# Kernel tuning notes

Measured on AMD Instinct MI355X. Metric: run time of the kernel, lower is better.

The kernel has to match this reference:

```python
import jax, jax.numpy as jnp
import numpy as np

N, E, B = 20000, 100000, 16
U_SZ, U_RED = 4096, 256
EDGE_H, EDGE_OUT = 1024, 512
NODE_H = 512
X_DIM, EA_DIM = 9, 1


def _lin(key, fan_out, fan_in):
    kw, kb = jax.random.split(key)
    s = 1.0 / np.sqrt(fan_in)
    w = jax.random.uniform(kw, (fan_out, fan_in), jnp.float32, -s, s)
    b = jax.random.uniform(kb, (fan_out,), jnp.float32, -s, s)
    return w, b


def setup_inputs() -> dict:
    key = jax.random.key(0)
    ks = jax.random.split(key, 16)
    inp = {}
    inp["x"] = jax.random.normal(ks[0], (N, X_DIM), jnp.float32)
    inp["edge_index"] = jax.random.randint(ks[1], (2, E), 0, N, jnp.int64)
    inp["edge_attr"] = jax.random.normal(ks[2], (E, EA_DIM), jnp.float32)
    inp["u"] = jax.random.normal(ks[3], (B, U_SZ), jnp.float32)
    inp["batch"] = jnp.sort(jax.random.randint(ks[4], (N,), 0, B, jnp.int64))
    # select_dim_reduction: Linear(4096, 256)
    inp["w_sel"], inp["b_sel"] = _lin(ks[5], U_RED, U_SZ)
    # edge MLP: 275 -> 1024 -> 1024 -> 1024 -> 1024 -> 512
    e_in = EA_DIM + 2 * X_DIM + U_RED  # 275
    inp["ew0"], inp["eb0"] = _lin(ks[6], EDGE_H, e_in)
    inp["ew1"], inp["eb1"] = _lin(ks[7], EDGE_H, EDGE_H)
    inp["ew2"], inp["eb2"] = _lin(ks[8], EDGE_H, EDGE_H)
    inp["ew3"], inp["eb3"] = _lin(ks[9], EDGE_H, EDGE_H)
    inp["ew4"], inp["eb4"] = _lin(ks[10], EDGE_OUT, EDGE_H)
    # node_mlp_1: (9+512) -> 512 -> 512 (relu after each)
    inp["nw0"], inp["nb0"] = _lin(ks[11], NODE_H, X_DIM + EDGE_OUT)
    inp["nw1"], inp["nb1"] = _lin(ks[12], NODE_H, NODE_H)
    # node_mlp_2: (9+512+256) -> 512 -> 1
    inp["mw0"], inp["mb0"] = _lin(ks[13], NODE_H, X_DIM + NODE_H + U_RED)
    inp["mw1"], inp["mb1"] = _lin(ks[14], 1, NODE_H)
    return inp


def reference(x, edge_index, edge_attr, u, batch,
              w_sel, b_sel,
              ew0, eb0, ew1, eb1, ew2, eb2, ew3, eb3, ew4, eb4,
              nw0, nb0, nw1, nb1, mw0, mb0, mw1, mb1):
    row, col = edge_index[0], edge_index[1]
    u_r = u @ w_sel.T + b_sel                       # [B, 256]
    eb_idx = batch[row]                             # edge -> graph
    # EdgeModel: cat([src, dest, edge_attr, u[batch]]) -> MLP
    e_in = jnp.concatenate([x[row], x[col], edge_attr, u_r[eb_idx]], axis=1)  # [E,275]
    h = jax.nn.relu(e_in @ ew0.T + eb0)
    h = jax.nn.relu(h @ ew1.T + eb1)
    h = jax.nn.relu(h @ ew2.T + eb2)
    h = jax.nn.relu(h @ ew3.T + eb3)
    edge_out = h @ ew4.T + eb4                      # [E, 512]
    # NodeModel: gather x[col], edge MLP, scatter_mean onto row
    n_in = jnp.concatenate([x[col], edge_out], axis=1)  # [E, 521]
    h = jax.nn.relu(n_in @ nw0.T + nb0)
    h = jax.nn.relu(h @ nw1.T + nb1)                # [E, 512]
    seg_sum = jax.ops.segment_sum(h, row, num_segments=x.shape[0])
    cnt = jax.ops.segment_sum(jnp.ones((h.shape[0],), h.dtype), row, num_segments=x.shape[0])
    agg = seg_sum / jnp.maximum(cnt, 1.0)[:, None]  # scatter_mean
    m_in = jnp.concatenate([x, agg, u_r[batch]], axis=1)  # [N, 777]
    h2 = jax.nn.relu(m_in @ mw0.T + mb0)
    out = h2 @ mw1.T + mb1                          # [N, 1]
    return jnp.squeeze(out)
```

## Files before the change

### kernel.cpp

```cpp
#include <hip/hip_runtime.h>


#define NN 20000
#define EE 100000
#define BB 16

typedef _Float16 f16x8 __attribute__((ext_vector_type(8)));
typedef _Float16 f16x4 __attribute__((ext_vector_type(4)));
typedef float f32x4 __attribute__((ext_vector_type(4)));

__device__ __forceinline__ int clampi(int v, int hi) {
    return v < 0 ? 0 : (v >= hi ? hi - 1 : v);
}

__device__ __forceinline__ void gld_lds16(const void* g, void* l) {
    __builtin_amdgcn_global_load_lds(
        (const __attribute__((address_space(1))) unsigned int*)g,
        (__attribute__((address_space(3))) unsigned int*)l, 16, 0, 0);
}

__global__ __launch_bounds__(512, 2) void gemm256(
    const _Float16* __restrict__ Ag, const _Float16* __restrict__ Wt,
    int KT, int KTs, const float* __restrict__ bias,
    _Float16* __restrict__ C, int KTo, int ktOff)
{
    __shared__ _Float16 As[32768];
    __shared__ _Float16 Bs[32768];

    const int tid  = threadIdx.x;
    const int lane = tid & 63;
    const int wid  = tid >> 6;
    const int wm = wid & 1;
    const int wn = wid >> 1;
    const int l15 = lane & 15;
    const int l4  = (lane >> 4) << 2;

    const int nb = gridDim.x;
    const int MT2 = gridDim.y;
    int f = blockIdx.y * nb + blockIdx.x;
    const int MT8 = MT2 & ~7;
    int p, c;
    if (f < MT8 * nb) {
        c = (f >> 3) % nb;
        p = (f & 7) + 8 * ((f >> 3) / nb);
    } else {
        int g = f - MT8 * nb;
        p = MT8 + g / nb;
        c = g % nb;
    }

    const int KTT = KT >> 1;
    const size_t soff = (size_t)tid * 8;
    const int doff = (tid & ~63) * 8;
    const int aoff = wm * 4096 + ((lane >> 4) << 10) + l15 * 8;
    const int boff = (wn >> 1) * 4096 + ((lane >> 4) << 10)
                   + ((wn & 1) * 64 + l15) * 8;

    auto stageA = [&](int tn, int s) {
        const size_t kk = (size_t)(2 * tn + s);
        const _Float16* g0 = Ag + ((size_t)(2 * p)     * KTs + kk) * 4096 + soff;
        const _Float16* g1 = Ag + ((size_t)(2 * p + 1) * KTs + kk) * 4096 + soff;
        _Float16* d = As + ((tn & 1) << 14) + (s << 13) + doff;
        gld_lds16(g0, d);
        gld_lds16(g1, d + 4096);
    };
    auto stageB = [&](int tn, int s) {
        const size_t kk = (size_t)(2 * tn + s);
        const _Float16* g0 = Wt + ((size_t)(2 * c)     * KT + kk) * 4096 + soff;
        const _Float16* g1 = Wt + ((size_t)(2 * c + 1) * KT + kk) * 4096 + soff;
        _Float16* d = Bs + ((tn & 1) << 14) + (s << 13) + doff;
        gld_lds16(g0, d);
        gld_lds16(g1, d + 4096);
    };

    f32x4 acc[8][4];
#pragma unroll
    for (int i = 0; i < 8; ++i)
#pragma unroll
        for (int j = 0; j < 4; ++j) acc[i][j] = (f32x4){0.f, 0.f, 0.f, 0.f};

    stageA(0, 0); stageB(0, 0); stageA(0, 1); stageB(0, 1);

    for (int t = 0; t < KTT; ++t) {
        const int pb = (t & 1) << 14;
#pragma unroll
        for (int sub = 0; sub < 2; ++sub) {
            if (t == KTT - 1 && sub == 1)
                asm volatile("s_waitcnt vmcnt(0)" ::: "memory");
            else
                asm volatile("s_waitcnt vmcnt(4)" ::: "memory");
            __builtin_amdgcn_s_barrier();
            const _Float16* Asub = As + pb + (sub << 13) + aoff;
            const _Float16* Bsub = Bs + pb + (sub << 13) + boff;
            f16x8 af[8], bf[4];
#pragma unroll
            for (int j = 0; j < 4; ++j) bf[j] = *(const f16x8*)(Bsub + j * 128);
#pragma unroll
            for (int i = 0; i < 8; ++i) af[i] = *(const f16x8*)(Asub + i * 128);
            if (t + 1 < KTT) { stageA(t + 1, sub); stageB(t + 1, sub); }
            __builtin_amdgcn_s_setprio(1);
#pragma unroll
            for (int i = 0; i < 8; ++i)
#pragma unroll
                for (int j = 0; j < 4; ++j)
                    acc[i][j] = __builtin_amdgcn_mfma_f32_16x16x32_f16(
                        af[i], bf[j], acc[i][j], 0, 0, 0);
            __builtin_amdgcn_s_setprio(0);
        }
    }

    _Float16* tr = As;
#pragma unroll
    for (int pass = 0; pass < 4; ++pass) {
        __syncthreads();
        if (wm == (pass >> 1)) {
            const int fi = (pass & 1) << 2;
#pragma unroll
            for (int i = 0; i < 4; ++i) {
#pragma unroll
                for (int v = 0; v < 4; ++v) {
                    const int lr = i * 16 + l4 + v;
#pragma unroll
                    for (int j = 0; j < 4; ++j) {
                        const int cc = wn * 64 + j * 16 + l15;
                        float val = acc[fi + i][j][v] + bias[c * 256 + cc];
                        val = fmaxf(val, 0.f);
                        tr[lr * 264 + cc] = (_Float16)val;
                    }
                }
            }
        }
        __syncthreads();
#pragma unroll
        for (int it = 0; it < 4; ++it) {
            const int id = it * 512 + tid;
            const int r  = id & 63;
            const int cg = id >> 6;
            f16x8 v8 = *(const f16x8*)(tr + r * 264 + cg * 8);
            const int kt = ktOff + c * 8 + (cg >> 2);
            const int mt_out = 2 * p + (pass >> 1);
            const int r128 = ((pass & 1) << 6) + r;
            *(f16x8*)(C + (((size_t)mt_out * KTo + kt) * 4 + (cg & 3)) * 1024
                        + (size_t)r128 * 8) = v8;
        }
    }
}

__global__ __launch_bounds__(256, 3) void gemmAD(
    const _Float16* __restrict__ Ag, const _Float16* __restrict__ Wt,
    int KT, int KTs, const float* __restrict__ bias,
    _Float16* __restrict__ C, int KTo, int ktOff)
{
    __shared__ _Float16 As[16384];

    const int tid  = threadIdx.x;
    const int lane = tid & 63;
    const int wid  = tid >> 6;
    const int wm = (wid & 1) << 6;
    const int wn = (wid >> 1) << 6;
    const int l15 = lane & 15;
    const int l4  = (lane >> 4) << 2;
    const int kg  = (lane >> 4) << 10;

    const int nb = gridDim.x;
    const int MT = gridDim.y;
    int f = blockIdx.y * nb + blockIdx.x;
    const int MT8 = MT & ~7;
    int p, c;
    if (f < MT8 * nb) {
        c = (f >> 3) % nb;
        p = (f & 7) + 8 * ((f >> 3) / nb);
    } else {
        int g = f - MT8 * nb;
        p = MT8 + g / nb;
        c = g % nb;
    }

    f32x4 acc[4][4];
#pragma unroll
    for (int i = 0; i < 4; ++i)
#pragma unroll
        for (int j = 0; j < 4; ++j) acc[i][j] = (f32x4){0.f, 0.f, 0.f, 0.f};

    const _Float16* gA = Ag + (size_t)p * KTs * 4096;
    const _Float16* gB = Wt + ((size_t)c * KT) * 4096 + kg + (wn + l15) * 8;
    const int ktLim = KT - 1;

    auto stageA = [&](int ktA) {
        const _Float16* s = gA + (size_t)ktA * 4096 + tid * 8;
        _Float16* d = As + ((ktA & 3) << 12) + wid * 512;
        gld_lds16(s, d);
        gld_lds16(s + 2048, d + 2048);
    };

    f16x8 bfA[4], bfB[4];
    auto loadB = [&](f16x8 (&bf)[4], int ktB) {
        const _Float16* bp = gB + (size_t)ktB * 4096;
#pragma unroll
        for (int j = 0; j < 4; ++j) bf[j] = *(const f16x8*)(bp + j * 128);
    };

    stageA(0);
    stageA(1 <= ktLim ? 1 : ktLim);
    loadB(bfA, 0);

    auto body = [&](int kt, f16x8 (&cur)[4], f16x8 (&nxt)[4]) {
        const int ktB = kt + 1 <= ktLim ? kt + 1 : ktLim;
        const int ktA = kt + 2 <= ktLim ? kt + 2 : ktLim;
        loadB(nxt, ktB);
        stageA(ktA);
        asm volatile("s_waitcnt vmcnt(12)" ::: "memory");
        __builtin_amdgcn_s_barrier();
        asm volatile("" ::: "memory");
        const _Float16* Ap = As + ((kt & 3) << 12) + kg + (wm + l15) * 8;
        f16x8 af[4];
#pragma unroll
        for (int i = 0; i < 4; ++i) af[i] = *(const f16x8*)(Ap + i * 128);
        __builtin_amdgcn_s_setprio(1);
#pragma unroll
        for (int i = 0; i < 4; ++i)
#pragma unroll
            for (int j = 0; j < 4; ++j)
                acc[i][j] = __builtin_amdgcn_mfma_f32_16x16x32_f16(
                    af[i], cur[j], acc[i][j], 0, 0, 0);
        __builtin_amdgcn_s_setprio(0);
    };

    for (int kt = 0; kt + 2 <= KT; kt += 2) {
        body(kt,     bfA, bfB);
        body(kt + 1, bfB, bfA);
    }
    if (KT & 1) body(KT - 1, bfA, bfB);

    _Float16* tr = As;
#pragma unroll
    for (int pass = 0; pass < 2; ++pass) {
        __syncthreads();
        if (wm == pass * 64) {
#pragma unroll
            for (int i = 0; i < 4; ++i) {
#pragma unroll
                for (int v = 0; v < 4; ++v) {
                    const int lr = i * 16 + l4 + v;
#pragma unroll
                    for (int j = 0; j < 4; ++j) {
                        const int cc = wn + j * 16 + l15;
                        float val = acc[i][j][v] + bias[c * 128 + cc];
                        val = fmaxf(val, 0.f);
                        tr[lr * 132 + cc] = (_Float16)val;
                    }
                }
            }
        }
        __syncthreads();
#pragma unroll
        for (int it = 0; it < 4; ++it) {
            const int id = it * 256 + tid;
            const int r  = id & 63;
            const int cg = id >> 6;
            f16x4 lo = *(const f16x4*)(tr + r * 132 + cg * 8);
            f16x4 hi = *(const f16x4*)(tr + r * 132 + cg * 8 + 4);
            f16x8 v8;
#pragma unroll
            for (int t = 0; t < 4; ++t) { v8[t] = lo[t]; v8[t + 4] = hi[t]; }
            const int kti = ktOff + (c << 2) + (cg >> 2);
            const int gr  = pass * 64 + r;
            size_t o = (((size_t)p * KTo + kti) * 4 + (cg & 3)) * 1024 + (size_t)gr * 8;
            *(f16x8*)(C + o) = v8;
        }
    }
}

template <int MODE>
__global__ __launch_bounds__(256, 4) void gemm_blk(
    const _Float16* __restrict__ A,
    const _Float16* __restrict__ Wt,
    int KT, int KTs,
    const float* __restrict__ bias, int ldbias, const int* __restrict__ gbid,
    void* __restrict__ C, int KTo, int ktOff,
    int ldc,
    const int* __restrict__ srow, float* __restrict__ aux,
    int M, int relu)
{
    __shared__ char smem[32768];
    _Float16* As = (_Float16*)smem;
    _Float16* Bs = As + 8192;

    const int tid  = threadIdx.x;
    const int lane = tid & 63;
    const int wid  = tid >> 6;
    const int wm = (wid & 1) << 6;
    const int wn = (wid >> 1) << 6;

    const int nb = gridDim.x;
    const int MT = gridDim.y;
    int f = blockIdx.y * nb + blockIdx.x;
    const int MT8 = MT & ~7;
    int p, c;
    if (f < MT8 * nb) {
        c = (f >> 3) % nb;
        p = (f & 7) + 8 * ((f >> 3) / nb);
    } else {
        int g = f - MT8 * nb;
        p = MT8 + g / nb;
        c = g % nb;
    }

    f32x4 acc[4][4];
#pragma unroll
    for (int i = 0; i < 4; ++i)
#pragma unroll
        for (int j = 0; j < 4; ++j) acc[i][j] = (f32x4){0.f, 0.f, 0.f, 0.f};

    const _Float16* pA = A + (size_t)p * KTs * 4096;
    const _Float16* pB = Wt + (size_t)c * KT * 4096;
    const int cb0 = wid * 64;
    const int cb1 = 256 + wid * 64;
    const int kq  = (lane >> 4) * 128;
    const int l15 = lane & 15;
    const int l4  = (lane >> 4) << 2;

    int kt = 0;
    for (; kt + 2 <= KT; kt += 2) {
        __syncthreads();
        gld_lds16(pA + (size_t)(cb0 + lane) * 8,        As + cb0 * 8);
        gld_lds16(pA + (size_t)(cb1 + lane) * 8,        As + cb1 * 8);
        gld_lds16(pA + 4096 + (size_t)(cb0 + lane) * 8, As + 4096 + cb0 * 8);
        gld_lds16(pA + 4096 + (size_t)(cb1 + lane) * 8, As + 4096 + cb1 * 8);
        gld_lds16(pB + (size_t)(cb0 + lane) * 8,        Bs + cb0 * 8);
        gld_lds16(pB + (size_t)(cb1 + lane) * 8,        Bs + cb1 * 8);
        gld_lds16(pB + 4096 + (size_t)(cb0 + lane) * 8, Bs + 4096 + cb0 * 8);
        gld_lds16(pB + 4096 + (size_t)(cb1 + lane) * 8, Bs + 4096 + cb1 * 8);
        pA += 8192; pB += 8192;
        __syncthreads();

#pragma unroll
        for (int s = 0; s < 2; ++s) {
            f16x8 af[4], bf[4];
            const int sb = s * 4096;
#pragma unroll
            for (int i = 0; i < 4; ++i)
                af[i] = *(const f16x8*)(As + sb + (size_t)((kq + wm + i * 16 + l15) << 3));
#pragma unroll
            for (int j = 0; j < 4; ++j)
                bf[j] = *(const f16x8*)(Bs + sb + (size_t)((kq + wn + j * 16 + l15) << 3));
#pragma unroll
            for (int i = 0; i < 4; ++i)
#pragma unroll
                for (int j = 0; j < 4; ++j)
                    acc[i][j] = __builtin_amdgcn_mfma_f32_16x16x32_f16(af[i], bf[j], acc[i][j], 0, 0, 0);
        }
    }
    if (kt < KT) {
        __syncthreads();
        gld_lds16(pA + (size_t)(cb0 + lane) * 8, As + cb0 * 8);
        gld_lds16(pA + (size_t)(cb1 + lane) * 8, As + cb1 * 8);
        gld_lds16(pB + (size_t)(cb0 + lane) * 8, Bs + cb0 * 8);
        gld_lds16(pB + (size_t)(cb1 + lane) * 8, Bs + cb1 * 8);
        __syncthreads();
        f16x8 af[4], bf[4];
#pragma unroll
        for (int i = 0; i < 4; ++i)
            af[i] = *(const f16x8*)(As + (size_t)((kq + wm + i * 16 + l15) << 3));
#pragma unroll
        for (int j = 0; j < 4; ++j)
            bf[j] = *(const f16x8*)(Bs + (size_t)((kq + wn + j * 16 + l15) << 3));
#pragma unroll
        for (int i = 0; i < 4; ++i)
#pragma unroll
            for (int j = 0; j < 4; ++j)
                acc[i][j] = __builtin_amdgcn_mfma_f32_16x16x32_f16(af[i], bf[j], acc[i][j], 0, 0, 0);
    }

    if (MODE == 0) {
        _Float16* tr = (_Float16*)smem;
#pragma unroll
        for (int pass = 0; pass < 2; ++pass) {
            __syncthreads();
            if (wm == pass * 64) {
#pragma unroll
                for (int i = 0; i < 4; ++i) {
#pragma unroll
                    for (int v = 0; v < 4; ++v) {
                        const int lr = i * 16 + l4 + v;
                        const float* brow = bias;
                        if (gbid) {
                            int m = p * 128 + pass * 64 + lr;
                            if (m >= M) m = M - 1;
                            brow = bias + (size_t)clampi(gbid[m], BB) * ldbias;
                        }
#pragma unroll
                        for (int j = 0; j < 4; ++j) {
                            const int cc = wn + j * 16 + l15;
                            float val = acc[i][j][v] + brow[c * 128 + cc];
                            if (relu) val = fmaxf(val, 0.f);
                            tr[lr * 132 + cc] = (_Float16)val;
                        }
                    }
                }
            }
            __syncthreads();
#pragma unroll
            for (int it = 0; it < 4; ++it) {
                const int id = it * 256 + tid;
                const int r  = id & 63;
                const int cg = id >> 6;
                f16x4 lo = *(const f16x4*)(tr + r * 132 + cg * 8);
                f16x4 hi = *(const f16x4*)(tr + r * 132 + cg * 8 + 4);
                f16x8 v8;
#pragma unroll
                for (int t = 0; t < 4; ++t) { v8[t] = lo[t]; v8[t + 4] = hi[t]; }
                const int kti = ktOff + (c << 2) + (cg >> 2);
                const int gr  = pass * 64 + r;
                size_t o = (((size_t)p * KTo + kti) * 4 + (cg & 3)) * 1024 + (size_t)gr * 8;
                *(f16x8*)((_Float16*)C + o) = v8;
            }
        }
    } else if (MODE == 1) {
#pragma unroll
        for (int i = 0; i < 4; ++i) {
#pragma unroll
            for (int v = 0; v < 4; ++v) {
                const int m = p * 128 + wm + i * 16 + l4 + v;
                if (m >= M) continue;
                const float* brow = bias;
                if (gbid) brow = bias + (size_t)clampi(gbid[m], BB) * ldbias;
#pragma unroll
                for (int j = 0; j < 4; ++j) {
                    const int col = c * 128 + wn + j * 16 + l15;
                    float val = acc[i][j][v] + brow[col];
                    if (relu) val = fmaxf(val, 0.f);
                    ((float*)C)[(size_t)m * ldc + col] = val;
                }
            }
        }
    } else if (MODE == 2) {
        float* trf = (float*)smem;
#pragma unroll
        for (int pass = 0; pass < 4; ++pass) {
            __syncthreads();
            if (wm == ((pass >> 1) << 6)) {
                const int i0 = (pass & 1) << 1;
#pragma unroll
                for (int ii = 0; ii < 2; ++ii) {
                    const int i = i0 + ii;
                    const int lr = ii * 16 + l4;
#pragma unroll
                    for (int v = 0; v < 4; ++v) {
#pragma unroll
                        for (int j = 0; j < 4; ++j) {
                            const int cc = wn + j * 16 + l15;
                            float val = acc[i][j][v] + bias[c * 128 + cc];
                            if (relu) val = fmaxf(val, 0.f);
                            trf[(lr + v) * 130 + cc] = val;
                        }
                    }
                }
            }
            __syncthreads();
            const int ebase = p * 128 + pass * 32;
#pragma unroll
            for (int it = 0; it < 16; ++it) {
                const int id = it * 256 + tid;
                const int lr = id >> 7;
                const int colg = id & 127;
                const int el = ebase + lr;
                if (el < M) {
                    const int node = clampi(srow[el], NN);
                    atomicAdd(&aux[(size_t)node * 512 + c * 128 + colg],
                              trf[lr * 130 + colg]);
                }
            }
        }
    } else {
        const float* mw1 = aux;
        float* out = (float*)C;
#pragma unroll
        for (int i = 0; i < 4; ++i) {
#pragma unroll
            for (int v = 0; v < 4; ++v) {
                const int m = p * 128 + wm + i * 16 + l4 + v;
                const int mc = m < M ? m : M - 1;
                const float* brow = bias + (size_t)clampi(gbid[mc], BB) * ldbias;
                float s = 0.f;
#pragma unroll
                for (int j = 0; j < 4; ++j) {
                    const int col = c * 128 + wn + j * 16 + l15;
                    float val = acc[i][j][v] + brow[col];
                    val = fmaxf(val, 0.f);
                    s += val * mw1[col];
                }
                s += __shfl_down(s, 8, 16);
                s += __shfl_down(s, 4, 16);
                s += __shfl_down(s, 2, 16);
                s += __shfl_down(s, 1, 16);
                if (l15 == 0 && m < M) atomicAdd(&out[m], s);
            }
        }
    }
}


__global__ void k_w2h_blk(const float* __restrict__ src, _Float16* __restrict__ dst,
                          int N, int Ksrc, int Kd, int mode)
{
    int t = blockIdx.x * blockDim.x + threadIdx.x;
    if (t >= N * Kd) return;
    int n = t / Kd, k = t - n * Kd;
    float v = 0.f;
    if (mode == 0)      { if (k < Ksrc) v = src[(size_t)n * Ksrc + k]; }
    else if (mode == 1) { if (k < 19) v = src[(size_t)n * 275 + k]; }
    else if (mode == 2) { if (k < 9) v = src[(size_t)n * Ksrc + k];
                          else if (k >= 32 && k < 544) v = src[(size_t)n * Ksrc + 9 + (k - 32)]; }
    else if (mode == 4) { if (k < Ksrc) v = src[(size_t)k * N + n]; }
    else                { v = src[(size_t)n * Ksrc + 9 + k]; }
    int KT = Kd >> 5;
    int nt = n >> 7, r = n & 127, kt = k >> 5, kg = (k >> 3) & 3, ko = k & 7;
    dst[(((size_t)nt * KT + kt) * 4 + kg) * 1024 + (size_t)r * 8 + ko] = (_Float16)v;
}

__global__ void k_fill_w32(const float* __restrict__ nw0, _Float16* __restrict__ whnc)
{
    int t = blockIdx.x * blockDim.x + threadIdx.x;
    if (t >= 512 * 32) return;
    int n = t >> 5, k = t & 31;
    float v = (k < 9) ? nw0[(size_t)n * 521 + k] : 0.f;
    int nt = n >> 7, r = n & 127, kg = (k >> 3) & 3, ko = k & 7;
    whnc[(((size_t)nt * 33 + 32) * 4 + kg) * 1024 + (size_t)r * 8 + ko] = (_Float16)v;
}

__global__ void k_bfuse(const float* __restrict__ nw0, const float* __restrict__ eb4,
                        const float* __restrict__ nb0, float* __restrict__ bf)
{
    int wave = (blockIdx.x * 256 + threadIdx.x) >> 6;
    int lane = threadIdx.x & 63;
    if (wave >= 512) return;
    const float* wr = nw0 + (size_t)wave * 521 + 9;
    float s = 0.f;
#pragma unroll
    for (int i = 0; i < 8; ++i) s += wr[lane * 8 + i] * eb4[lane * 8 + i];
    for (int off = 32; off; off >>= 1) s += __shfl_down(s, off);
    if (lane == 0) bf[wave] = s + nb0[wave];
}

__global__ void k_u_r(const float* __restrict__ u, const float* __restrict__ w_sel,
                      const float* __restrict__ b_sel, float* __restrict__ u_r)
{
    int wave = (blockIdx.x * 256 + threadIdx.x) >> 6;
    int lane = threadIdx.x & 63;
    int b = wave >> 8, n = wave & 255;
    const float4* u4 = (const float4*)(u + (size_t)b * 4096);
    const float4* w4 = (const float4*)(w_sel + (size_t)n * 4096);
    float s = 0.f;
    for (int i = lane; i < 1024; i += 64) {
        float4 a = u4[i], c = w4[i];
        s += a.x * c.x + a.y * c.y + a.z * c.z + a.w * c.w;
    }
    for (int off = 32; off; off >>= 1) s += __shfl_down(s, off);
    if (lane == 0) u_r[b * 256 + n] = s + b_sel[n];
}

__global__ void k_graph_bias(const float* __restrict__ u_r, const float* __restrict__ w,
                             const float* __restrict__ b, float* __restrict__ ub,
                             int Nout, int Ksrc, int koff)
{
    int wave = (blockIdx.x * 256 + threadIdx.x) >> 6;
    int lane = threadIdx.x & 63;
    if (wave >= 16 * Nout) return;
    int g = wave / Nout, n = wave - g * Nout;
    const float* ur = u_r + (size_t)g * 256;
    const float* wr = w + (size_t)n * Ksrc + koff;
    float s = 0.f;
#pragma unroll
    for (int i = 0; i < 4; ++i) s += ur[lane * 4 + i] * wr[lane * 4 + i];
    for (int off = 32; off; off >>= 1) s += __shfl_down(s, off);
    if (lane == 0) ub[(size_t)g * Nout + n] = s + b[n];
}

__global__ void k_gbe(const int* __restrict__ row, const int* __restrict__ batch,
                      int* __restrict__ gbe, float* __restrict__ cnt)
{
    int e = blockIdx.x * blockDim.x + threadIdx.x;
    if (e >= EE) return;
    int r = clampi(row[e], NN);
    gbe[e] = clampi(batch[r], BB);
    atomicAdd(&cnt[r], 1.f);
}

__global__ void k_init_out(float* __restrict__ out, const float* __restrict__ mb1)
{
    int t = blockIdx.x * blockDim.x + threadIdx.x;
    if (t < NN) out[t] = mb1[0];
}

__global__ void k_gather_edge_blk(const float* __restrict__ x, const float* __restrict__ ea,
                                  const int* __restrict__ row, const int* __restrict__ col,
                                  _Float16* __restrict__ dst, _Float16* __restrict__ pong,
                                  int e0, int ec, int MTR)
{
    int t = blockIdx.x * blockDim.x + threadIdx.x;
    if (t >= MTR * 4) return;
    int r = t >> 2, kg = t & 3;
    int e = e0 + r; int emax = e0 + ec - 1;
    if (e > emax) e = emax;
    int ri = clampi(row[e], NN), ci = clampi(col[e], NN);
    f16x8 v;
    f16x8 vx = (f16x8)(_Float16)0.f;
#pragma unroll
    for (int j = 0; j < 8; ++j) {
        int cc = kg * 8 + j;
        float fv = 0.f;
        if (cc < 9)       fv = x[(size_t)ri * 9 + cc];
        else if (cc < 18) fv = x[(size_t)ci * 9 + (cc - 9)];
        else if (cc == 18) fv = ea[e];
        v[j] = (_Float16)fv;
        if (cc < 9) vx[j] = (_Float16)x[(size_t)ci * 9 + cc];
    }
    *(f16x8*)(dst + (size_t)(r >> 7) * 4096 + (size_t)kg * 1024 + (size_t)(r & 127) * 8) = v;
    *(f16x8*)(pong + (((size_t)(r >> 7) * 33 + 32) * 4 + kg) * 1024 + (size_t)(r & 127) * 8) = vx;
}

__global__ void k_gather_min(const float* __restrict__ x, const float* __restrict__ agg,
                             const float* __restrict__ cnt, _Float16* __restrict__ dst, int MTR)
{
    int t = blockIdx.x * blockDim.x + threadIdx.x;
    if (t >= MTR * 68) return;
    int r = t / 68, q = t - r * 68;
    int kt = q >> 2, kg = q & 3;
    int n = r < NN ? r : NN - 1;
    f16x8 v = (f16x8)(_Float16)0.f;
    if (kt == 0) {
#pragma unroll
        for (int j = 0; j < 8; ++j) {
            int cc = kg * 8 + j;
            if (cc < 9) v[j] = (_Float16)x[(size_t)n * 9 + cc];
        }
    } else {
        float inv = 1.f / fmaxf(cnt[n], 1.f);
        int cbase = (kt - 1) * 32 + kg * 8;
        const float4* ap = (const float4*)(agg + (size_t)n * 512 + cbase);
        float4 a0 = ap[0], a1 = ap[1];
        v[0] = (_Float16)(a0.x * inv); v[1] = (_Float16)(a0.y * inv);
        v[2] = (_Float16)(a0.z * inv); v[3] = (_Float16)(a0.w * inv);
        v[4] = (_Float16)(a1.x * inv); v[5] = (_Float16)(a1.y * inv);
        v[6] = (_Float16)(a1.z * inv); v[7] = (_Float16)(a1.w * inv);
    }
    *(f16x8*)(dst + ((size_t)(r >> 7) * 17 + kt) * 4096 + (size_t)kg * 1024 + (size_t)(r & 127) * 8) = v;
}


#define GRID1(n) dim3(((n) + 255) / 256)

static inline void gemmB0(hipStream_t s, const _Float16* A, const _Float16* Wt, int KT, int KTs,
                          const float* bias, int ldbias, const int* gbid,
                          void* C, int KTo, int ktOff,
                          int M, int MT, int NT, int relu)
{
    hipLaunchKernelGGL(gemm_blk<0>, dim3(NT, MT), dim3(256), 0, s,
                       A, Wt, KT, KTs, bias, ldbias, gbid, C, KTo, ktOff, 0,
                       nullptr, nullptr, M, relu);
}
static inline void gemmB2(hipStream_t s, const _Float16* A, const _Float16* Wt, int KT, int KTs,
                          const float* bias, const int* srow, float* agg,
                          int M, int MT, int NT, int relu)
{
    hipLaunchKernelGGL(gemm_blk<2>, dim3(NT, MT), dim3(256), 0, s,
                       A, Wt, KT, KTs, bias, 0, nullptr, nullptr, 0, 0, 0,
                       srow, agg, M, relu);
}
static inline void gemmB3(hipStream_t s, const _Float16* A, const _Float16* Wt, int KT, int KTs,
                          const float* bias, int ldbias, const int* gbid,
                          float* out, const float* mw1,
                          int M, int MT, int NT)
{
    hipLaunchKernelGGL(gemm_blk<3>, dim3(NT, MT), dim3(256), 0, s,
                       A, Wt, KT, KTs, bias, ldbias, gbid, out, 0, 0, 0,
                       nullptr, (float*)mw1, M, 1);
}

extern "C" void kernel_launch(void* const* d_in, const int* in_sizes, int n_in,
                              void* d_out, int out_size, void* d_ws, size_t ws_size,
                              hipStream_t stream)
{
    const float* x     = (const float*)d_in[0];
    const int*   ei    = (const int*)d_in[1];
    const float* ea    = (const float*)d_in[2];
    const float* u     = (const float*)d_in[3];
    const int*   batch = (const int*)d_in[4];
    const float* w_sel = (const float*)d_in[5];
    const float* b_sel = (const float*)d_in[6];
    const float* ew0 = (const float*)d_in[7];   const float* eb0 = (const float*)d_in[8];
    const float* ew1 = (const float*)d_in[9];   const float* eb1 = (const float*)d_in[10];
    const float* ew2 = (const float*)d_in[11];  const float* eb2 = (const float*)d_in[12];
    const float* ew3 = (const float*)d_in[13];  const float* eb3 = (const float*)d_in[14];
    const float* ew4 = (const float*)d_in[15];  const float* eb4 = (const float*)d_in[16];
    const float* nw0 = (const float*)d_in[17];  const float* nb0 = (const float*)d_in[18];
    const float* nw1 = (const float*)d_in[19];  const float* nb1 = (const float*)d_in[20];
    const float* mw0 = (const float*)d_in[21];  const float* mb0 = (const float*)d_in[22];
    const float* mw1 = (const float*)d_in[23];  const float* mb1 = (const float*)d_in[24];

    const int* row = ei;
    const int* col = ei + EE;

    char* W = (char*)d_ws;
    size_t off = 0;
    auto alloc = [&](size_t bytes) -> char* {
        char* p = W + off;
        off = (off + bytes + 255) & ~(size_t)255;
        return p;
    };
    float*    cnt   = (float*)alloc(20000 * 4);
    float*    agg   = (float*)alloc((size_t)NN * 512 * 4);
    float*    zbias = (float*)alloc(1024 * 4);
    const size_t zeroBytes = off;
    float*    u_r  = (float*)alloc(16 * 256 * 4);
    float*    ub0  = (float*)alloc(16 * 1024 * 4);
    float*    ubm  = (float*)alloc(16 * 512 * 4);
    float*    bfu  = (float*)alloc(512 * 4);
    int*      gbe  = (int*)alloc((size_t)EE * 4);
    _Float16* wh0   = (_Float16*)alloc((size_t)8 * 1 * 4096 * 2);
    _Float16* wh1   = (_Float16*)alloc((size_t)8 * 32 * 4096 * 2);
    _Float16* wh2   = (_Float16*)alloc((size_t)8 * 32 * 4096 * 2);
    _Float16* wh3   = (_Float16*)alloc((size_t)8 * 32 * 4096 * 2);
    _Float16* whnc  = (_Float16*)alloc((size_t)4 * 33 * 4096 * 2);
    _Float16* whn1  = (_Float16*)alloc((size_t)4 * 16 * 4096 * 2);
    _Float16* whm0  = (_Float16*)alloc((size_t)4 * 17 * 4096 * 2);
    _Float16* nw0eoB= (_Float16*)alloc((size_t)4 * 16 * 4096 * 2);
    _Float16* ew4T  = (_Float16*)alloc((size_t)8 * 16 * 4096 * 2);
    const int MTm = (NN + 127) / 128;
    _Float16* m_in = (_Float16*)alloc((size_t)MTm * 17 * 4096 * 2);
    const size_t fixedBytes = off;

    static const int ecOpts[] = {32768, 25000, 12500, 10000, 5000};
    int EC = 5000;
    for (int i = 0; i < 5; ++i) {
        int ec = ecOpts[i];
        size_t MTRc = (size_t)((ec + 255) / 256) * 256;
        size_t need = fixedBytes + MTRc * 64 + 2 * (MTRc * 2112) + 4096;
        if (need <= ws_size) { EC = ec; break; }
    }
    const bool big = (EC == 32768);
    const size_t MTR = (size_t)((EC + 255) / 256) * 256;
    _Float16* e_in = (_Float16*)alloc(MTR * 64);
    _Float16* ping = (_Float16*)alloc(MTR * 2112);
    _Float16* pong = (_Float16*)alloc(MTR * 2112);
    const int NCH = (EE + EC - 1) / EC;

    (void)hipMemsetAsync(W, 0, zeroBytes, stream);
    hipLaunchKernelGGL(k_init_out, GRID1(NN), dim3(256), 0, stream, (float*)d_out, mb1);

    hipLaunchKernelGGL(k_u_r, dim3(1024), dim3(256), 0, stream, u, w_sel, b_sel, u_r);
    hipLaunchKernelGGL(k_graph_bias, GRID1(16 * 1024 * 64), dim3(256), 0, stream,
                       u_r, ew0, eb0, ub0, 1024, 275, 19);
    hipLaunchKernelGGL(k_graph_bias, GRID1(16 * 512 * 64), dim3(256), 0, stream,
                       u_r, mw0, mb0, ubm, 512, 777, 521);
    hipLaunchKernelGGL(k_gbe, GRID1(EE), dim3(256), 0, stream, row, batch, gbe, cnt);
    hipLaunchKernelGGL(k_bfuse, dim3(128), dim3(256), 0, stream, nw0, eb4, nb0, bfu);

    auto pack = [&](const float* w, _Float16* wh, int N, int Ksrc, int Kd, int mode) {
        hipLaunchKernelGGL(k_w2h_blk, GRID1(N * Kd), dim3(256), 0, stream, w, wh, N, Ksrc, Kd, mode);
    };
    pack(ew0, wh0, 1024, 275, 32, 1);
    pack(ew1, wh1, 1024, 1024, 1024, 0);
    pack(ew2, wh2, 1024, 1024, 1024, 0);
    pack(ew3, wh3, 1024, 1024, 1024, 0);
    pack(nw1, whn1, 512, 512, 512, 0);
    pack(mw0, whm0, 512, 777, 544, 2);
    pack(nw0, nw0eoB, 512, 521, 512, 5);
    pack(ew4, ew4T, 1024, 512, 512, 4);
    gemmB0(stream, nw0eoB, ew4T, 16, 16, zbias, 0, nullptr, whnc, 33, 0, 512, 4, 8, 0);
    hipLaunchKernelGGL(k_fill_w32, GRID1(512 * 32), dim3(256), 0, stream, nw0, whnc);

    for (int ch = 0; ch < NCH; ++ch) {
        int e0 = ch * EC;
        int ec = EC; if (e0 + ec > EE) ec = EE - e0;
        const int ecr  = ((ec + 255) / 256) * 256;
        const int MTc  = ecr / 128;
        const int MT2c = ecr / 256;
        hipLaunchKernelGGL(k_gather_edge_blk, GRID1(ecr * 4), dim3(256), 0, stream,
                           x, ea, row, col, e_in, pong, e0, ec, ecr);
        gemmB0(stream, e_in, wh0, 1, 1, ub0, 1024, gbe + e0, ping, 33, 0, ec, MTc, 8, 1);
        auto wideL = [&](const _Float16* Ain, const _Float16* Wt,
                         const float* b, _Float16* Cout) {
            if (big)
                hipLaunchKernelGGL(gemm256, dim3(4, MT2c), dim3(512), 0, stream,
                                   Ain, Wt, 32, 33, b, Cout, 33, 0);
            else
                hipLaunchKernelGGL(gemmAD, dim3(8, MTc), dim3(256), 0, stream,
                                   Ain, Wt, 32, 33, b, Cout, 33, 0);
        };
        wideL(ping, wh1, eb1, pong);
        wideL(pong, wh2, eb2, ping);
        wideL(ping, wh3, eb3, pong);
        hipLaunchKernelGGL(gemmAD, dim3(4, MTc), dim3(256), 0, stream,
                           pong, whnc, 33, 33, bfu, ping, 16, 0);
        gemmB2(stream, ping, whn1, 16, 16, nb1, row + e0, agg, ec, MTc, 4, 1);
    }

    hipLaunchKernelGGL(k_gather_min, GRID1((int)(MTm * 128) * 68), dim3(256), 0, stream,
                       x, agg, cnt, m_in, MTm * 128);
    gemmB3(stream, m_in, whm0, 17, 17, ubm, 512, batch, (float*)d_out, mw1, NN, MTm, 4);
}
```

Before: 1.478 ms.

## Restructure GEMM main loop into 4-slot ring with register prefetch of next fragments

Replaces the double-buffered two-substep loop with a per-k-step phase over a 4-slot LDS ring, issuing global-to-LDS loads two steps ahead. The A and B fragments for the next step are read from LDS while the current step's MFMAs run, using ping-pong B registers, so LDS read latency overlaps with matrix math. This raises register pressure and assumes KT is even, since the loop steps by two with no remainder handling.

Measured after the change: 1.499 ms. About the same (+1.4%).

```diff
diff --git a/kernel.cpp b/kernel.cpp
--- a/kernel.cpp
+++ b/kernel.cpp
@@ -49,64 +49,75 @@
         c = g % nb;
     }
 
-    const int KTT = KT >> 1;
+    const int S = KT;
     const size_t soff = (size_t)tid * 8;
     const int doff = (tid & ~63) * 8;
     const int aoff = wm * 4096 + ((lane >> 4) << 10) + l15 * 8;
     const int boff = (wn >> 1) * 4096 + ((lane >> 4) << 10)
                    + ((wn & 1) * 64 + l15) * 8;
 
-    auto stageA = [&](int tn, int s) {
-        const size_t kk = (size_t)(2 * tn + s);
-        const _Float16* g0 = Ag + ((size_t)(2 * p)     * KTs + kk) * 4096 + soff;
-        const _Float16* g1 = Ag + ((size_t)(2 * p + 1) * KTs + kk) * 4096 + soff;
-        _Float16* d = As + ((tn & 1) << 14) + (s << 13) + doff;
-        gld_lds16(g0, d);
-        gld_lds16(g1, d + 4096);
+    auto stage = [&](int ph) {
+        const _Float16* gA0 = Ag + ((size_t)(2 * p)     * KTs + ph) * 4096 + soff;
+        const _Float16* gA1 = Ag + ((size_t)(2 * p + 1) * KTs + ph) * 4096 + soff;
+        const _Float16* gB0 = Wt + ((size_t)(2 * c)     * KT  + ph) * 4096 + soff;
+        const _Float16* gB1 = Wt + ((size_t)(2 * c + 1) * KT  + ph) * 4096 + soff;
+        _Float16* dA = As + ((ph & 3) << 13) + doff;
+        _Float16* dB = Bs + ((ph & 3) << 13) + doff;
+        gld_lds16(gA0, dA); gld_lds16(gA1, dA + 4096);
+        gld_lds16(gB0, dB); gld_lds16(gB1, dB + 4096);
     };
-    auto stageB = [&](int tn, int s) {
-        const size_t kk = (size_t)(2 * tn + s);
-        const _Float16* g0 = Wt + ((size_t)(2 * c)     * KT + kk) * 4096 + soff;
-        const _Float16* g1 = Wt + ((size_t)(2 * c + 1) * KT + kk) * 4096 + soff;
-        _Float16* d = Bs + ((tn & 1) << 14) + (s << 13) + doff;
-        gld_lds16(g0, d);
-        gld_lds16(g1, d + 4096);
+
+    f32x4 acc[8][4];
+#pragma unroll
+    for (int i = 0; i < 8; ++i)
+#pragma unroll
+        for (int j = 0; j < 4; ++j) acc[i][j] = (f32x4){0.f, 0.f, 0.f, 0.f};
+
+    f16x8 af[8], bfA[4], bfB[4];
+
+    stage(0); stage(1);
+    asm volatile("s_waitcnt vmcnt(4)" ::: "memory");
+    __builtin_amdgcn_s_barrier();
+    {
+        const _Float16* A0 = As + aoff;
+        const _Float16* B0 = Bs + boff;
+#pragma unroll
+        for (int j = 0; j < 4; ++j) bfA[j] = *(const f16x8*)(B0 + j * 128);
+#pragma unroll
+        for (int i = 0; i < 8; ++i) af[i] = *(const f16x8*)(A0 + i * 128);
+    }
+
+    auto phase = [&](int s, f16x8 (&cur)[4], f16x8 (&nxt)[4]) {
+        if (s + 2 < S) {
+            stage(s + 2);
+            asm volatile("s_waitcnt vmcnt(4)" ::: "memory");
+        } else {
+            asm volatile("s_waitcnt vmcnt(0)" ::: "memory");
+        }
+        __builtin_amdgcn_s_barrier();
+        const bool more = (s + 1 < S);
+        const int r1 = ((s + 1) & 3) << 13;
+        const _Float16* An = As + r1 + aoff;
+        const _Float16* Bn = Bs + r1 + boff;
+        if (more) {
+#pragma unroll
+            for (int j = 0; j < 4; ++j) nxt[j] = *(const f16x8*)(Bn + j * 128);
+        }
+        __builtin_amdgcn_s_setprio(1);
+#pragma unroll
+        for (int i = 0; i < 8; ++i) {
+#pragma unroll
+            for (int j = 0; j < 4; ++j)
+                acc[i][j] = __builtin_amdgcn_mfma_f32_16x16x32_f16(
+                    af[i], cur[j], acc[i][j], 0, 0, 0);
+            if (more) af[i] = *(const f16x8*)(An + i * 128);
+        }
+        __builtin_amdgcn_s_setprio(0);
     };
 
-    f32x4 acc[8][4];
-#pragma unroll
-    for (int i = 0; i < 8; ++i)
-#pragma unroll
-        for (int j = 0; j < 4; ++j) acc[i][j] = (f32x4){0.f, 0.f, 0.f, 0.f};
-
-    stageA(0, 0); stageB(0, 0); stageA(0, 1); stageB(0, 1);
-
-    for (int t = 0; t < KTT; ++t) {
-        const int pb = (t & 1) << 14;
-#pragma unroll
-        for (int sub = 0; sub < 2; ++sub) {
-            if (t == KTT - 1 && sub == 1)
-                asm volatile("s_waitcnt vmcnt(0)" ::: "memory");
-            else
-                asm volatile("s_waitcnt vmcnt(4)" ::: "memory");
-            __builtin_amdgcn_s_barrier();
-            const _Float16* Asub = As + pb + (sub << 13) + aoff;
-            const _Float16* Bsub = Bs + pb + (sub << 13) + boff;
-            f16x8 af[8], bf[4];
-#pragma unroll
-            for (int j = 0; j < 4; ++j) bf[j] = *(const f16x8*)(Bsub + j * 128);
-#pragma unroll
-            for (int i = 0; i < 8; ++i) af[i] = *(const f16x8*)(Asub + i * 128);
-            if (t + 1 < KTT) { stageA(t + 1, sub); stageB(t + 1, sub); }
-            __builtin_amdgcn_s_setprio(1);
-#pragma unroll
-            for (int i = 0; i < 8; ++i)
-#pragma unroll
-                for (int j = 0; j < 4; ++j)
-                    acc[i][j] = __builtin_amdgcn_mfma_f32_16x16x32_f16(
-                        af[i], bf[j], acc[i][j], 0, 0, 0);
-            __builtin_amdgcn_s_setprio(0);
-        }
+    for (int s = 0; s + 2 <= S; s += 2) {
+        phase(s,     bfA, bfB);
+        phase(s + 1, bfB, bfA);
     }
 
     _Float16* tr = As;
```

## Replace 256x256 wide-layer GEMM with 256x128 tile, 256-thread kernel

Applied to the files above, without the earlier changes.

The wide edge-MLP layers now use a 256x128 output tile computed by 4 waves instead of a 256x256 tile over 8 waves. The kernel stages one K-slab per step with a simple double buffer in 48KB of LDS, and the epilogue transposes through a narrower padded LDS tile. Smaller LDS use and blocks allow more concurrent blocks and a grid twice as wide. In exchange, each tile reuses fetched data less, and every step now waits for all loads to finish (vmcnt(0)), so there is less load/compute overlap.

After: 1.381 ms. -6.6%, faster.

```diff
diff --git a/kernel.cpp b/kernel.cpp
--- a/kernel.cpp
+++ b/kernel.cpp
@@ -19,23 +19,23 @@
         (__attribute__((address_space(3))) unsigned int*)l, 16, 0, 0);
 }
 
-__global__ __launch_bounds__(512, 2) void gemm256(
+__global__ __launch_bounds__(256, 2) void gemm256h(
     const _Float16* __restrict__ Ag, const _Float16* __restrict__ Wt,
     int KT, int KTs, const float* __restrict__ bias,
     _Float16* __restrict__ C, int KTo, int ktOff)
 {
-    __shared__ _Float16 As[32768];
-    __shared__ _Float16 Bs[32768];
+    __shared__ _Float16 smem[24576];
 
     const int tid  = threadIdx.x;
     const int lane = tid & 63;
     const int wid  = tid >> 6;
-    const int wm = wid & 1;
-    const int wn = wid >> 1;
-    const int l15 = lane & 15;
-    const int l4  = (lane >> 4) << 2;
-
-    const int nb = gridDim.x;
+    const int wm   = wid & 1;
+    const int wn   = wid >> 1;
+    const int l15  = lane & 15;
+    const int l4   = (lane >> 4) << 2;
+    const int kq   = (lane >> 4) << 10;
+
+    const int nb  = gridDim.x;
     const int MT2 = gridDim.y;
     int f = blockIdx.y * nb + blockIdx.x;
     const int MT8 = MT2 & ~7;
@@ -49,29 +49,20 @@
         c = g % nb;
     }
 
-    const int KTT = KT >> 1;
-    const size_t soff = (size_t)tid * 8;
-    const int doff = (tid & ~63) * 8;
-    const int aoff = wm * 4096 + ((lane >> 4) << 10) + l15 * 8;
-    const int boff = (wn >> 1) * 4096 + ((lane >> 4) << 10)
-                   + ((wn & 1) * 64 + l15) * 8;
-
-    auto stageA = [&](int tn, int s) {
-        const size_t kk = (size_t)(2 * tn + s);
-        const _Float16* g0 = Ag + ((size_t)(2 * p)     * KTs + kk) * 4096 + soff;
-        const _Float16* g1 = Ag + ((size_t)(2 * p + 1) * KTs + kk) * 4096 + soff;
-        _Float16* d = As + ((tn & 1) << 14) + (s << 13) + doff;
-        gld_lds16(g0, d);
-        gld_lds16(g1, d + 4096);
+    const int S = KT;
+    auto stage = [&](int ph) {
+        const _Float16* gA0 = Ag + ((size_t)(2 * p)     * KTs + ph) * 4096 + tid * 8;
+        const _Float16* gA1 = Ag + ((size_t)(2 * p + 1) * KTs + ph) * 4096 + tid * 8;
+        const _Float16* gB  = Wt + ((size_t)c * KT + ph) * 4096 + tid * 8;
+        _Float16* rA = smem + (ph & 1) * 12288;
+        _Float16* rB = rA + 8192;
+        gld_lds16(gA0,        rA + wid * 512);
+        gld_lds16(gA0 + 2048, rA + 2048 + wid * 512);
+        gld_lds16(gA1,        rA + 4096 + wid * 512);
+        gld_lds16(gA1 + 2048, rA + 6144 + wid * 512);
+        gld_lds16(gB,         rB + wid * 512);
+        gld_lds16(gB + 2048,  rB + 2048 + wid * 512);
     };
-    auto stageB = [&](int tn, int s) {
-        const size_t kk = (size_t)(2 * tn + s);
-        const _Float16* g0 = Wt + ((size_t)(2 * c)     * KT + kk) * 4096 + soff;
-        const _Float16* g1 = Wt + ((size_t)(2 * c + 1) * KT + kk) * 4096 + soff;
-        _Float16* d = Bs + ((tn & 1) << 14) + (s << 13) + doff;
-        gld_lds16(g0, d);
-        gld_lds16(g1, d + 4096);
-    };
 
     f32x4 acc[8][4];
 #pragma unroll
@@ -79,37 +70,32 @@
 #pragma unroll
         for (int j = 0; j < 4; ++j) acc[i][j] = (f32x4){0.f, 0.f, 0.f, 0.f};
 
-    stageA(0, 0); stageB(0, 0); stageA(0, 1); stageB(0, 1);
-
-    for (int t = 0; t < KTT; ++t) {
-        const int pb = (t & 1) << 14;
-#pragma unroll
-        for (int sub = 0; sub < 2; ++sub) {
-            if (t == KTT - 1 && sub == 1)
-                asm volatile("s_waitcnt vmcnt(0)" ::: "memory");
-            else
-                asm volatile("s_waitcnt vmcnt(4)" ::: "memory");
-            __builtin_amdgcn_s_barrier();
-            const _Float16* Asub = As + pb + (sub << 13) + aoff;
-            const _Float16* Bsub = Bs + pb + (sub << 13) + boff;
-            f16x8 af[8], bf[4];
-#pragma unroll
-            for (int j = 0; j < 4; ++j) bf[j] = *(const f16x8*)(Bsub + j * 128);
-#pragma unroll
-            for (int i = 0; i < 8; ++i) af[i] = *(const f16x8*)(Asub + i * 128);
-            if (t + 1 < KTT) { stageA(t + 1, sub); stageB(t + 1, sub); }
-            __builtin_amdgcn_s_setprio(1);
-#pragma unroll
-            for (int i = 0; i < 8; ++i)
-#pragma unroll
-                for (int j = 0; j < 4; ++j)
-                    acc[i][j] = __builtin_amdgcn_mfma_f32_16x16x32_f16(
-                        af[i], bf[j], acc[i][j], 0, 0, 0);
-            __builtin_amdgcn_s_setprio(0);
-        }
-    }
-
-    _Float16* tr = As;
+    stage(0);
+
+    for (int s = 0; s < S; ++s) {
+        asm volatile("s_waitcnt vmcnt(0)" ::: "memory");
+        __builtin_amdgcn_s_barrier();
+        if (s + 1 < S) stage(s + 1);
+        const _Float16* rA = smem + (s & 1) * 12288;
+        const _Float16* rB = rA + 8192;
+        const _Float16* Ap = rA + wm * 4096 + kq + l15 * 8;
+        const _Float16* Bp = rB + kq + wn * 512 + l15 * 8;
+        f16x8 af[8], bf[4];
+#pragma unroll
+        for (int j = 0; j < 4; ++j) bf[j] = *(const f16x8*)(Bp + j * 128);
+#pragma unroll
+        for (int i = 0; i < 8; ++i) af[i] = *(const f16x8*)(Ap + i * 128);
+        __builtin_amdgcn_s_setprio(1);
+#pragma unroll
+        for (int i = 0; i < 8; ++i)
+#pragma unroll
+            for (int j = 0; j < 4; ++j)
+                acc[i][j] = __builtin_amdgcn_mfma_f32_16x16x32_f16(
+                    af[i], bf[j], acc[i][j], 0, 0, 0);
+        __builtin_amdgcn_s_setprio(0);
+    }
+
+    _Float16* tr = smem;
 #pragma unroll
     for (int pass = 0; pass < 4; ++pass) {
         __syncthreads();
@@ -123,9 +109,9 @@
 #pragma unroll
                     for (int j = 0; j < 4; ++j) {
                         const int cc = wn * 64 + j * 16 + l15;
-                        float val = acc[fi + i][j][v] + bias[c * 256 + cc];
+                        float val = acc[fi + i][j][v] + bias[c * 128 + cc];
                         val = fmaxf(val, 0.f);
-                        tr[lr * 264 + cc] = (_Float16)val;
+                        tr[lr * 132 + cc] = (_Float16)val;
                     }
                 }
             }
@@ -133,14 +119,18 @@
         __syncthreads();
 #pragma unroll
         for (int it = 0; it < 4; ++it) {
-            const int id = it * 512 + tid;
+            const int id = it * 256 + tid;
             const int r  = id & 63;
             const int cg = id >> 6;
-            f16x8 v8 = *(const f16x8*)(tr + r * 264 + cg * 8);
-            const int kt = ktOff + c * 8 + (cg >> 2);
+            f16x4 lo = *(const f16x4*)(tr + r * 132 + cg * 8);
+            f16x4 hi = *(const f16x4*)(tr + r * 132 + cg * 8 + 4);
+            f16x8 v8;
+#pragma unroll
+            for (int t = 0; t < 4; ++t) { v8[t] = lo[t]; v8[t + 4] = hi[t]; }
+            const int kti = ktOff + (c << 2) + (cg >> 2);
             const int mt_out = 2 * p + (pass >> 1);
             const int r128 = ((pass & 1) << 6) + r;
-            *(f16x8*)(C + (((size_t)mt_out * KTo + kt) * 4 + (cg & 3)) * 1024
+            *(f16x8*)(C + (((size_t)mt_out * KTo + kti) * 4 + (cg & 3)) * 1024
                         + (size_t)r128 * 8) = v8;
         }
     }
@@ -783,7 +773,7 @@
         auto wideL = [&](const _Float16* Ain, const _Float16* Wt,
                          const float* b, _Float16* Cout) {
             if (big)
-                hipLaunchKernelGGL(gemm256, dim3(4, MT2c), dim3(512), 0, stream,
+                hipLaunchKernelGGL(gemm256h, dim3(8, MT2c), dim3(256), 0, stream,
                                    Ain, Wt, 32, 33, b, Cout, 33, 0);
             else
                 hipLaunchKernelGGL(gemmAD, dim3(8, MTc), dim3(256), 0, stream,
```
